# Performance work log

Measured on AMD Instinct MI355X. Metric: run time of the kernel, lower is better.

## Reference

```python
import jax, jax.numpy as jnp
import numpy as np

B, CIN, HALF, H, W = 4, 3, 32, 512, 512
K_MODE, PAD_MODE, N_LEVELS = 11, 5, 17  # 11x11 mode window, reflect pad 5, round(x*255/16) in 0..16
SLOPE, EPS = 0.01, 1e-5


def _leaky(x):
    return jnp.where(x > 0, x, SLOPE * x)


def _bn(x, g, b):
    # BatchNorm2d in training mode: batch statistics over (B,H,W), biased var
    m = x.mean(axis=(0, 2, 3), keepdims=True)
    v = x.var(axis=(0, 2, 3), keepdims=True)
    return (x - m) * jax.lax.rsqrt(v + EPS) * g[None, :, None, None] + b[None, :, None, None]


def _mode_pool(x):
    # quantize to 17 discrete levels, then sliding-window histogram mode (fused
    # equivalent of unfold + torch.mode; argmax first-hit == smallest tied value)
    k = jnp.clip(jnp.round(x * (255.0 / 16.0)), 0, N_LEVELS - 1).astype(jnp.int32)
    kp = jnp.pad(k, ((0, 0), (0, 0), (PAD_MODE, PAD_MODE), (PAD_MODE, PAD_MODE)), mode='reflect')
    onehot = (kp[..., None] == jnp.arange(N_LEVELS, dtype=jnp.int32)).astype(jnp.float32)
    counts = jax.lax.reduce_window(onehot, 0.0, jax.lax.add,
                                   (1, 1, K_MODE, K_MODE, 1), (1, 1, 1, 1, 1), 'VALID')
    mode_k = jnp.argmax(counts, axis=-1)  # [B,C,H,W]
    return mode_k.astype(jnp.float32) * (16.0 / 256.0)


def _nearest(x, Ho, Wo):
    # torch interpolate(mode='nearest'): src = floor(dst * in/out)
    hi, wi = x.shape[2], x.shape[3]
    ri = (jnp.arange(Ho) * hi) // Ho
    ci = (jnp.arange(Wo) * wi) // Wo
    return x[:, :, ri][:, :, :, ci]


def _forward(x, w1, b1, w2, b2, bn1_g, bn1_b, w3, b3, bn2_g, bn2_b,
             k_down, k_w, bnw_g, bnw_b, k_h, bnh_g, bnh_b):
    xm = _mode_pool(x)  # [B,CIN,H,W]
    # prepare: 1x1 conv -> LeakyReLU -> 1x1 conv -> BN -> LeakyReLU -> depthwise 1x1 -> BN -> LeakyReLU
    h = _leaky(jnp.einsum('bchw,oc->bohw', xm, w1) + b1[None, :, None, None])
    h = jnp.einsum('bchw,oc->bohw', h, w2) + b2[None, :, None, None]
    h = _leaky(_bn(h, bn1_g, bn1_b))
    h = h * w3[None, :, None, None] + b3[None, :, None, None]  # groups=half 1x1 conv
    h = _leaky(_bn(h, bn2_g, bn2_b))
    Bs, half, Ho, Wo = h.shape
    score = jnp.zeros((Bs, 2 * half, Ho, Wo), jnp.float32)
    d = h
    while min(d.shape[2], d.shape[3]) >= 3:  # static pyramid: 512->171->57->19->7->3->1
        d = jax.lax.conv_general_dilated(d, k_down, (3, 3), ((1, 1), (1, 1)),
                                         dimension_numbers=('NCHW', 'OIHW', 'NCHW'),
                                         feature_group_count=half)
        z = _nearest(d, Ho, Wo)
        wbr = _leaky(_bn(z * k_w[None, :, None, None], bnw_g, bnw_b))  # width branch (SharedConv k=1, no bias)
        hbr = _leaky(_bn(z * k_h[None, :, None, None], bnh_g, bnh_b))  # height branch
        # stack(dim=1).reshape => width channels first, then height channels
        score = score + jnp.concatenate([wbr, hbr], axis=1)
    return score


def setup_inputs():
    key = jax.random.key(0)
    ks = jax.random.split(key, 8)
    x = jax.random.uniform(ks[0], (B, CIN, H, W), dtype=jnp.float32)
    s1, s2 = 1.0 / np.sqrt(CIN), 1.0 / np.sqrt(2 * CIN)
    return {
        'x': x,
        'w1': jax.random.uniform(ks[1], (2 * CIN, CIN), jnp.float32, -s1, s1),
        'b1': jax.random.uniform(ks[2], (2 * CIN,), jnp.float32, -s1, s1),
        'w2': jax.random.uniform(ks[3], (HALF, 2 * CIN), jnp.float32, -s2, s2),
        'b2': jax.random.uniform(ks[4], (HALF,), jnp.float32, -s2, s2),
        'bn1_g': jnp.ones((HALF,), jnp.float32),
        'bn1_b': jnp.zeros((HALF,), jnp.float32),
        'w3': jax.random.uniform(ks[5], (HALF,), jnp.float32, -1.0, 1.0),
        'b3': jax.random.uniform(ks[6], (HALF,), jnp.float32, -1.0, 1.0),
        'bn2_g': jnp.ones((HALF,), jnp.float32),
        'bn2_b': jnp.zeros((HALF,), jnp.float32),
        'k_down': jnp.full((HALF, 1, 3, 3), 0.5, jnp.float32),  # SharedConv init
        'k_w': jnp.full((HALF,), 0.5, jnp.float32),
        'bnw_g': jnp.ones((HALF,), jnp.float32),
        'bnw_b': jnp.zeros((HALF,), jnp.float32),
        'k_h': jnp.full((HALF,), 0.5, jnp.float32),
        'bnh_g': jnp.ones((HALF,), jnp.float32),
        'bnh_b': jnp.zeros((HALF,), jnp.float32),
    }


def reference(x, w1, b1, w2, b2, bn1_g, bn1_b, w3, b3, bn2_g, bn2_b,
              k_down, k_w, bnw_g, bnw_b, k_h, bnh_g, bnh_b):
    return _forward(x, w1, b1, w2, b2, bn1_g, bn1_b, w3, b3, bn2_g, bn2_b,
                    k_down, k_w, bnw_g, bnw_b, k_h, bnh_g, bnh_b)
```

## Files before the change

kernel.cpp:

```cpp
#include <hip/hip_runtime.h>

#define HH 512
#define WW 512
#define HW 262144
#define NPIX 1048576
#define NPIXF 1048576.0f

typedef float f4 __attribute__((ext_vector_type(4)));

__device__ __forceinline__ float leaky(float v) { return v > 0.f ? v : 0.01f * v; }

__device__ __forceinline__ float repw(int i, int s) {
    return (float)(((i + 1) * 512 + s - 1) / s - (i * 512 + s - 1) / s);
}

__device__ __forceinline__ void hins(unsigned long long& h0, unsigned long long& h1,
                                     unsigned& c16, int val) {
    unsigned long long inc = 1ull << ((val & 7) * 8);
    h0 += (val < 8) ? inc : 0;
    h1 += (val >= 8 && val < 16) ? inc : 0;
    c16 += (unsigned)(val >> 4);
}
__device__ __forceinline__ void hrem(unsigned long long& h0, unsigned long long& h1,
                                     unsigned& c16, int val) {
    unsigned long long inc = 1ull << ((val & 7) * 8);
    h0 -= (val < 8) ? inc : 0;
    h1 -= (val >= 8 && val < 16) ? inc : 0;
    c16 -= (unsigned)(val >> 4);
}

__global__ __launch_bounds__(256) void mode_kernel(const float* __restrict__ x,
                                                   unsigned char* __restrict__ modeq) {
    __shared__ unsigned char q[26 * 272];
    __shared__ unsigned ch[2][267 * 5];
    const int plane = blockIdx.z;
    const int tc0 = blockIdx.x * 256;
    const int tr0 = blockIdx.y * 16;
    const float* xp = x + (size_t)plane * HW;
    for (int idx = threadIdx.x; idx < 26 * 266; idx += 256) {
        int r = idx / 266;
        int cc = idx - r * 266;
        int gr = tr0 + r - 5; gr = gr < 0 ? -gr : (gr > 511 ? 1022 - gr : gr);
        int gc = tc0 + cc - 5; gc = gc < 0 ? -gc : (gc > 511 ? 1022 - gc : gc);
        float v = rintf(xp[gr * WW + gc] * 15.9375f);
        v = fminf(fmaxf(v, 0.f), 16.f);
        q[r * 272 + cc] = (unsigned char)(int)v;
    }
    const int t = threadIdx.x;
    unsigned long long A0 = 0, A1 = 0; unsigned A2 = 0;
    unsigned long long B0 = 0, B1 = 0; unsigned B2 = 0;
    __syncthreads();
    for (int r = 0; r < 16; ++r) {
        if (r == 0) {
            #pragma unroll
            for (int v = 0; v < 11; ++v) {
                hins(A0, A1, A2, q[v * 272 + t]);
                if (t < 10) hins(B0, B1, B2, q[v * 272 + 256 + t]);
            }
        } else {
            hrem(A0, A1, A2, q[(r - 1) * 272 + t]);
            hins(A0, A1, A2, q[(r + 10) * 272 + t]);
            if (t < 10) {
                hrem(B0, B1, B2, q[(r - 1) * 272 + 256 + t]);
                hins(B0, B1, B2, q[(r + 10) * 272 + 256 + t]);
            }
        }
        unsigned* cb = ch[r & 1];
        cb[t * 5 + 0] = (unsigned)A0;
        cb[t * 5 + 1] = (unsigned)(A0 >> 32);
        cb[t * 5 + 2] = (unsigned)A1;
        cb[t * 5 + 3] = (unsigned)(A1 >> 32);
        cb[t * 5 + 4] = A2;
        if (t < 10) {
            cb[(256 + t) * 5 + 0] = (unsigned)B0;
            cb[(256 + t) * 5 + 1] = (unsigned)(B0 >> 32);
            cb[(256 + t) * 5 + 2] = (unsigned)B1;
            cb[(256 + t) * 5 + 3] = (unsigned)(B1 >> 32);
            cb[(256 + t) * 5 + 4] = B2;
        }
        __syncthreads();
        unsigned long long H0 = 0, H1 = 0; unsigned C = 0;
        #pragma unroll
        for (int v = 0; v < 11; ++v) {
            const unsigned* p = &cb[(t + v) * 5];
            H0 += (unsigned long long)p[0] | ((unsigned long long)p[1] << 32);
            H1 += (unsigned long long)p[2] | ((unsigned long long)p[3] << 32);
            C += p[4];
        }
        unsigned m = 0;
        #pragma unroll
        for (int i = 0; i < 8; ++i) {
            unsigned cnt = (unsigned)(H0 >> (8 * i)) & 0xFFu;
            unsigned val = (cnt << 8) | (unsigned)(16 - i);
            m = m > val ? m : val;
        }
        #pragma unroll
        for (int i = 8; i < 16; ++i) {
            unsigned cnt = (unsigned)(H1 >> (8 * (i - 8))) & 0xFFu;
            unsigned val = (cnt << 8) | (unsigned)(16 - i);
            m = m > val ? m : val;
        }
        unsigned val16 = (C << 8);
        m = m > val16 ? m : val16;
        int k = 16 - (int)(m & 0xFFu);
        modeq[(size_t)plane * HW + (size_t)(tr0 + r) * WW + tc0 + t] = (unsigned char)k;
    }
}

__global__ __launch_bounds__(256) void hist_kernel(const unsigned char* __restrict__ modeq,
                                                   const float* __restrict__ w1,
                                                   const float* __restrict__ b1,
                                                   unsigned* __restrict__ partial,
                                                   float* __restrict__ mom) {
    __shared__ unsigned lh[4913];
    __shared__ float mred[27][4];
    for (int i = threadIdx.x; i < 4913; i += 256) lh[i] = 0;
    __syncthreads();
    int base = blockIdx.x * 8192;
    int b = base >> 18;
    int hw0 = base & (HW - 1);
    const unsigned char* mp = modeq + (size_t)b * 3 * HW;
    #pragma unroll
    for (int j = 0; j < 8; ++j) {
        int g = threadIdx.x + 256 * j;
        int hw = hw0 + g * 4;
        unsigned u0 = *(const unsigned*)(mp + hw);
        unsigned u1 = *(const unsigned*)(mp + hw + HW);
        unsigned u2 = *(const unsigned*)(mp + hw + 2 * HW);
        #pragma unroll
        for (int k = 0; k < 4; ++k) {
            int k0 = (u0 >> (8 * k)) & 0xFF;
            int k1 = (u1 >> (8 * k)) & 0xFF;
            int k2 = (u2 >> (8 * k)) & 0xFF;
            atomicAdd(&lh[k0 + 17 * k1 + 289 * k2], 1u);
        }
    }
    __syncthreads();
    unsigned* pp = partial + blockIdx.x * 4913;
    for (int i = threadIdx.x; i < 4913; i += 256) pp[i] = lh[i];
    float w1r[18], b1r[6];
    #pragma unroll
    for (int k = 0; k < 18; ++k) w1r[k] = w1[k];
    #pragma unroll
    for (int o = 0; o < 6; ++o) b1r[o] = b1[o];
    float M[27];
    #pragma unroll
    for (int i = 0; i < 27; ++i) M[i] = 0.f;
    for (int bin = threadIdx.x; bin < 4913; bin += 256) {
        float cnt = (float)lh[bin];
        int k0 = bin % 17;
        int r = bin / 17;
        int k1 = r % 17;
        int k2 = r / 17;
        float xm0 = k0 * 0.0625f, xm1 = k1 * 0.0625f, xm2 = k2 * 0.0625f;
        float t1[6];
        #pragma unroll
        for (int o = 0; o < 6; ++o)
            t1[o] = leaky(xm0 * w1r[o * 3] + xm1 * w1r[o * 3 + 1] + xm2 * w1r[o * 3 + 2] + b1r[o]);
        #pragma unroll
        for (int o = 0; o < 6; ++o) M[o] += cnt * t1[o];
        int ii = 6;
        #pragma unroll
        for (int j = 0; j < 6; ++j)
            #pragma unroll
            for (int k = j; k < 6; ++k) { M[ii] += cnt * t1[j] * t1[k]; ++ii; }
    }
    int wv = threadIdx.x >> 6;
    #pragma unroll
    for (int i = 0; i < 27; ++i) {
        float v = M[i];
        #pragma unroll
        for (int off = 32; off >= 1; off >>= 1) v += __shfl_xor(v, off);
        if ((threadIdx.x & 63) == 0) mred[i][wv] = v;
    }
    __syncthreads();
    if (threadIdx.x < 27)
        atomicAdd(&mom[threadIdx.x],
                  mred[threadIdx.x][0] + mred[threadIdx.x][1] +
                  mred[threadIdx.x][2] + mred[threadIdx.x][3]);
}

__global__ __launch_bounds__(256) void redhist_kernel(const unsigned* __restrict__ partial,
                                                      float* __restrict__ histf) {
    int bin = blockIdx.x * 256 + threadIdx.x;
    if (bin >= 4913) return;
    unsigned s = 0;
    for (int blk = 0; blk < 128; ++blk) s += partial[blk * 4913 + bin];
    histf[bin] = (float)s;
}

__global__ void solveA_kernel(const float* __restrict__ mom, const float* __restrict__ w2,
                              const float* __restrict__ b2, const float* __restrict__ g1,
                              const float* __restrict__ bb1, float* __restrict__ p1) {
    int c = threadIdx.x;
    float w2r[6];
    #pragma unroll
    for (int k = 0; k < 6; ++k) w2r[k] = w2[c * 6 + k];
    float b2c = b2[c];
    float wm1 = 0.f;
    #pragma unroll
    for (int k = 0; k < 6; ++k) wm1 += w2r[k] * mom[k];
    float q = 0.f;
    int ii = 6;
    #pragma unroll
    for (int j = 0; j < 6; ++j)
        #pragma unroll
        for (int k = j; k < 6; ++k) {
            float f = w2r[j] * w2r[k] * mom[ii];
            q += (j == k) ? f : 2.f * f;
            ++ii;
        }
    float mean = b2c + wm1 / NPIXF;
    float ex2 = b2c * b2c + 2.f * b2c * (wm1 / NPIXF) + q / NPIXF;
    float var = ex2 - mean * mean;
    float a = g1[c] * rsqrtf(var + 1e-5f);
    p1[c] = a;
    p1[32 + c] = bb1[c] - mean * a;
}

__global__ __launch_bounds__(256) void solveB_kernel(const float* __restrict__ histf,
                                                     const float* __restrict__ w1,
                                                     const float* __restrict__ b1,
                                                     const float* __restrict__ w2,
                                                     const float* __restrict__ b2,
                                                     const float* __restrict__ p1,
                                                     float* __restrict__ tstats) {
    __shared__ float rs[8][32], rq[8][32];
    int c = threadIdx.x & 31;
    int sub = threadIdx.x >> 5;
    float w1r[18], b1r[6];
    #pragma unroll
    for (int k = 0; k < 18; ++k) w1r[k] = w1[k];
    #pragma unroll
    for (int o = 0; o < 6; ++o) b1r[o] = b1[o];
    float w2r[6];
    #pragma unroll
    for (int k = 0; k < 6; ++k) w2r[k] = w2[c * 6 + k];
    float b2c = b2[c];
    float a1 = p1[c], c1 = p1[32 + c];
    float sm = 0.f, sq = 0.f;
    for (int bin = blockIdx.x + 32 * sub; bin < 4913; bin += 256) {
        float cnt = histf[bin];
        int k0 = bin % 17;
        int r = bin / 17;
        int k1 = r % 17;
        int k2 = r / 17;
        float xm0 = k0 * 0.0625f, xm1 = k1 * 0.0625f, xm2 = k2 * 0.0625f;
        float t1[6];
        #pragma unroll
        for (int o = 0; o < 6; ++o)
            t1[o] = leaky(xm0 * w1r[o * 3] + xm1 * w1r[o * 3 + 1] + xm2 * w1r[o * 3 + 2] + b1r[o]);
        float h2 = b2c;
        #pragma unroll
        for (int k = 0; k < 6; ++k) h2 += w2r[k] * t1[k];
        float t = leaky(a1 * h2 + c1);
        sm += cnt * t;
        sq += cnt * t * t;
    }
    rs[sub][c] = sm; rq[sub][c] = sq;
    __syncthreads();
    if (threadIdx.x < 32) {
        float s = 0.f, qq = 0.f;
        #pragma unroll
        for (int g = 0; g < 8; ++g) { s += rs[g][threadIdx.x]; qq += rq[g][threadIdx.x]; }
        atomicAdd(&tstats[threadIdx.x], s);
        atomicAdd(&tstats[32 + threadIdx.x], qq);
    }
}

__global__ void fin2_kernel(const float* __restrict__ tstats, const float* __restrict__ w3,
                            const float* __restrict__ b3, const float* __restrict__ g,
                            const float* __restrict__ bb, float* __restrict__ p2) {
    int c = threadIdx.x;
    float mt = tstats[c] / NPIXF;
    float vt = tstats[32 + c] / NPIXF - mt * mt;
    float m2 = w3[c] * mt + b3[c];
    float v2 = w3[c] * w3[c] * vt;
    float a = g[c] * rsqrtf(v2 + 1e-5f);
    p2[c] = a;
    p2[32 + c] = bb[c] - m2 * a;
}

__global__ __launch_bounds__(64) void d1_kernel(const unsigned char* __restrict__ modeq,
                                                const float* __restrict__ w1,
                                                const float* __restrict__ b1,
                                                const float* __restrict__ w2,
                                                const float* __restrict__ b2,
                                                const float* __restrict__ w3,
                                                const float* __restrict__ b3,
                                                const float* __restrict__ p1,
                                                const float* __restrict__ p2,
                                                const float* __restrict__ kd,
                                                float* __restrict__ d1) {
    int j = blockIdx.x * 64 + threadIdx.x;
    if (j >= 171) return;
    int i = blockIdx.y;
    int b = blockIdx.z;
    float acc[32];
    #pragma unroll
    for (int c = 0; c < 32; ++c) acc[c] = 0.f;
    const unsigned char* mp = modeq + (size_t)b * 3 * HW;
    #pragma unroll
    for (int u = 0; u < 3; ++u) {
        int r = 3 * i - 1 + u;
        if (r < 0 || r > 511) continue;
        #pragma unroll
        for (int v = 0; v < 3; ++v) {
            int col = 3 * j - 1 + v;
            if (col < 0 || col > 511) continue;
            int off = r * WW + col;
            float xm0 = mp[off] * 0.0625f, xm1 = mp[off + HW] * 0.0625f, xm2 = mp[off + 2 * HW] * 0.0625f;
            float t1[6];
            #pragma unroll
            for (int o = 0; o < 6; ++o)
                t1[o] = leaky(xm0 * w1[o * 3] + xm1 * w1[o * 3 + 1] + xm2 * w1[o * 3 + 2] + b1[o]);
            #pragma unroll
            for (int c = 0; c < 32; ++c) {
                float h2 = b2[c];
                #pragma unroll
                for (int k = 0; k < 6; ++k) h2 += w2[c * 6 + k] * t1[k];
                float t = leaky(h2 * p1[c] + p1[32 + c]);
                float uu = t * w3[c] + b3[c];
                float hv = leaky(uu * p2[c] + p2[32 + c]);
                acc[c] += hv * kd[c * 9 + u * 3 + v];
            }
        }
    }
    size_t base = ((size_t)(b * 32) * 171 + i) * 171 + j;
    #pragma unroll
    for (int c = 0; c < 32; ++c) d1[base + (size_t)c * 29241] = acc[c];
}

__device__ __forceinline__ void red_atomic(float sm, float sq, float* rsc,
                                           float* lst, int c) {
    #pragma unroll
    for (int off = 32; off >= 1; off >>= 1) {
        sm += __shfl_xor(sm, off);
        sq += __shfl_xor(sq, off);
    }
    __syncthreads();
    int wv = threadIdx.x >> 6;
    if ((threadIdx.x & 63) == 0) { rsc[wv] = sm; rsc[8 + wv] = sq; }
    __syncthreads();
    if (threadIdx.x == 0) {
        atomicAdd(&lst[c], rsc[0] + rsc[1] + rsc[2] + rsc[3]);
        atomicAdd(&lst[32 + c], rsc[8] + rsc[9] + rsc[10] + rsc[11]);
    }
}

__device__ __forceinline__ void lvl(const float* src, int sin, float* dstL,
                                    float* dstG, int sout, const float* kreg,
                                    float* rsc, float* lst, int c) {
    float sm = 0.f, sq = 0.f;
    int n = sout * sout;
    for (int i = threadIdx.x; i < n; i += 256) {
        int oi = i / sout, oj = i - oi * sout;
        float acc = 0.f;
        #pragma unroll
        for (int u = 0; u < 3; ++u) {
            int r = 3 * oi - 1 + u;
            if ((unsigned)r >= (unsigned)sin) continue;
            #pragma unroll
            for (int v = 0; v < 3; ++v) {
                int cc = 3 * oj - 1 + v;
                if ((unsigned)cc >= (unsigned)sin) continue;
                acc += src[r * sin + cc] * kreg[u * 3 + v];
            }
        }
        dstG[i] = acc;
        if (dstL) dstL[i] = acc;
        float w = repw(oi, sout) * repw(oj, sout);
        sm += w * acc;
        sq += w * acc * acc;
    }
    red_atomic(sm, sq, rsc, lst, c);
}

__global__ __launch_bounds__(256) void pyramid_kernel(const float* __restrict__ d1,
                                                      float* __restrict__ d2,
                                                      float* __restrict__ d3,
                                                      float* __restrict__ d4,
                                                      float* __restrict__ d5,
                                                      float* __restrict__ d6,
                                                      const float* __restrict__ kd,
                                                      float* __restrict__ lstats) {
    __shared__ float buf2[3249];
    __shared__ float buf3[361];
    __shared__ float buf4[49];
    __shared__ float buf5[9];
    __shared__ float rsc[16];
    int bc = blockIdx.x;
    int c = bc & 31;
    float kreg[9];
    #pragma unroll
    for (int qq = 0; qq < 9; ++qq) kreg[qq] = kd[c * 9 + qq];
    const float* s1 = d1 + (size_t)bc * 29241;
    float sm = 0.f, sq = 0.f;
    for (int i = threadIdx.x; i < 29241; i += 256) {
        int oi = i / 171, oj = i - oi * 171;
        float w = repw(oi, 171) * repw(oj, 171);
        float v = s1[i];
        sm += w * v;
        sq += w * v * v;
    }
    red_atomic(sm, sq, rsc, &lstats[0 * 64], c);
    lvl(s1, 171, buf2, d2 + (size_t)bc * 3249, 57, kreg, rsc, &lstats[1 * 64], c);
    lvl(buf2, 57, buf3, d3 + (size_t)bc * 361, 19, kreg, rsc, &lstats[2 * 64], c);
    lvl(buf3, 19, buf4, d4 + (size_t)bc * 49, 7, kreg, rsc, &lstats[3 * 64], c);
    lvl(buf4, 7, buf5, d5 + (size_t)bc * 9, 3, kreg, rsc, &lstats[4 * 64], c);
    lvl(buf5, 3, nullptr, d6 + bc, 1, kreg, rsc, &lstats[5 * 64], c);
}

__global__ void fin3_kernel(const float* __restrict__ lstats, const float* __restrict__ kw,
                            const float* __restrict__ gw, const float* __restrict__ bw,
                            const float* __restrict__ kh, const float* __restrict__ gh,
                            const float* __restrict__ bh, float* __restrict__ lp) {
    int t = threadIdx.x;
    if (t >= 192) return;
    int l = t >> 5, c = t & 31;
    float mz = lstats[l * 64 + c] / NPIXF;
    float vz = lstats[l * 64 + 32 + c] / NPIXF - mz * mz;
    float kwc = kw[c];
    float aw = gw[c] * rsqrtf(kwc * kwc * vz + 1e-5f);
    float khc = kh[c];
    float ah = gh[c] * rsqrtf(khc * khc * vz + 1e-5f);
    float* o = lp + (size_t)(l * 32 + c) * 4;
    o[0] = kwc * aw;
    o[1] = bw[c] - kwc * mz * aw;
    o[2] = khc * ah;
    o[3] = bh[c] - khc * mz * ah;
}

__global__ __launch_bounds__(256) void final_kernel(const float* __restrict__ d1,
                                                    const float* __restrict__ d2,
                                                    const float* __restrict__ d3,
                                                    const float* __restrict__ d4,
                                                    const float* __restrict__ d5,
                                                    const float* __restrict__ d6,
                                                    const float* __restrict__ lp,
                                                    float* __restrict__ out) {
    int idx = blockIdx.x * 256 + threadIdx.x;
    int w4 = (idx & 127) << 2;
    int h = (idx >> 7) & 511;
    int c = (idx >> 16) & 31;
    int b = idx >> 21;
    const float* ds[6] = {d1, d2, d3, d4, d5, d6};
    const int ss[6] = {171, 57, 19, 7, 3, 1};
    float accw[4] = {0.f, 0.f, 0.f, 0.f};
    float acch[4] = {0.f, 0.f, 0.f, 0.f};
    #pragma unroll
    for (int l = 0; l < 6; ++l) {
        int s = ss[l];
        int sh = (h * s) >> 9;
        const float* base = ds[l] + ((size_t)(b * 32 + c) * s + sh) * s;
        const float* a = lp + (size_t)(l * 32 + c) * 4;
        float a0 = a[0], a1 = a[1], a2 = a[2], a3 = a[3];
        #pragma unroll
        for (int k = 0; k < 4; ++k) {
            int sw = ((w4 + k) * s) >> 9;
            float val = base[sw];
            accw[k] += leaky(val * a0 + a1);
            acch[k] += leaky(val * a2 + a3);
        }
    }
    size_t o = (((size_t)(b * 64 + c)) << 18) + ((size_t)h << 9) + w4;
    f4 vw = {accw[0], accw[1], accw[2], accw[3]};
    f4 vh = {acch[0], acch[1], acch[2], acch[3]};
    __builtin_nontemporal_store(vw, (f4*)(out + o));
    __builtin_nontemporal_store(vh, (f4*)(out + o + (((size_t)32) << 18)));
}

extern "C" void kernel_launch(void* const* d_in, const int* in_sizes, int n_in,
                              void* d_out, int out_size, void* d_ws, size_t ws_size,
                              hipStream_t stream) {
    const float* x     = (const float*)d_in[0];
    const float* w1    = (const float*)d_in[1];
    const float* b1    = (const float*)d_in[2];
    const float* w2    = (const float*)d_in[3];
    const float* b2    = (const float*)d_in[4];
    const float* bn1g  = (const float*)d_in[5];
    const float* bn1b  = (const float*)d_in[6];
    const float* w3    = (const float*)d_in[7];
    const float* b3    = (const float*)d_in[8];
    const float* bn2g  = (const float*)d_in[9];
    const float* bn2b  = (const float*)d_in[10];
    const float* kd    = (const float*)d_in[11];
    const float* kw    = (const float*)d_in[12];
    const float* bnwg  = (const float*)d_in[13];
    const float* bnwb  = (const float*)d_in[14];
    const float* kh    = (const float*)d_in[15];
    const float* bnhg  = (const float*)d_in[16];
    const float* bnhb  = (const float*)d_in[17];
    float* out = (float*)d_out;

    char* ws = (char*)d_ws;
    unsigned char* modeq = (unsigned char*)ws;
    float* lstats = (float*)(ws + 3145728);
    float* mom    = lstats + 384;
    float* tstats = mom + 32;
    float* p1 = (float*)(ws + 3145728 + 2048);
    float* p2 = p1 + 64;
    float* lp = p2 + 64;
    unsigned* partial = (unsigned*)(ws + 3151360);
    float* histf = (float*)(ws + 3151360 + 2515456);
    float* d1 = (float*)(ws + 3151360 + 2515456 + 20480);
    float* d2 = d1 + 3742848;
    float* d3 = d2 + 415872;
    float* d4 = d3 + 46208;
    float* d5 = d4 + 6272;
    float* d6 = d5 + 1152;

    hipMemsetAsync(lstats, 0, 2048, stream);

    mode_kernel<<<dim3(2, 32, 12), 256, 0, stream>>>(x, modeq);
    hist_kernel<<<128, 256, 0, stream>>>(modeq, w1, b1, partial, mom);
    redhist_kernel<<<20, 256, 0, stream>>>(partial, histf);
    solveA_kernel<<<1, 32, 0, stream>>>(mom, w2, b2, bn1g, bn1b, p1);
    solveB_kernel<<<32, 256, 0, stream>>>(histf, w1, b1, w2, b2, p1, tstats);
    fin2_kernel<<<1, 32, 0, stream>>>(tstats, w3, b3, bn2g, bn2b, p2);
    d1_kernel<<<dim3(3, 171, 4), 64, 0, stream>>>(modeq, w1, b1, w2, b2, w3, b3, p1, p2, kd, d1);
    pyramid_kernel<<<128, 256, 0, stream>>>(d1, d2, d3, d4, d5, d6, kd, lstats);
    fin3_kernel<<<1, 192, 0, stream>>>(lstats, kw, bnwg, bnwb, kh, bnhg, bnhb, lp);
    final_kernel<<<32768, 256, 0, stream>>>(d1, d2, d3, d4, d5, d6, lp, out);
}
```

Before: 469.6 us.

## Fuse joint histogram into mode kernel and replace atomics with partial buffers

The mode kernel now handles all three channels of a batch tile in one block. It builds the 3-channel joint histogram and first-moment partials directly, which removes the separate hist and redhist kernels and the re-read of modeq. Global float atomics and the memset are replaced by per-block partial buffers that are reduced in solveA, solveB, fin2 and fin3. The trade-off is that the mode kernel grid shrinks threefold with serial per-plane work, reducing parallelism and occupancy.

```diff
diff --git a/kernel.cpp b/kernel.cpp
--- a/kernel.cpp
+++ b/kernel.cpp
@@ -30,114 +30,105 @@
 }
 
 __global__ __launch_bounds__(256) void mode_kernel(const float* __restrict__ x,
-                                                   unsigned char* __restrict__ modeq) {
-    __shared__ unsigned char q[26 * 272];
-    __shared__ unsigned ch[2][267 * 5];
-    const int plane = blockIdx.z;
-    const int tc0 = blockIdx.x * 256;
-    const int tr0 = blockIdx.y * 16;
-    const float* xp = x + (size_t)plane * HW;
-    for (int idx = threadIdx.x; idx < 26 * 266; idx += 256) {
-        int r = idx / 266;
-        int cc = idx - r * 266;
-        int gr = tr0 + r - 5; gr = gr < 0 ? -gr : (gr > 511 ? 1022 - gr : gr);
-        int gc = tc0 + cc - 5; gc = gc < 0 ? -gc : (gc > 511 ? 1022 - gc : gc);
-        float v = rintf(xp[gr * WW + gc] * 15.9375f);
-        v = fminf(fmaxf(v, 0.f), 16.f);
-        q[r * 272 + cc] = (unsigned char)(int)v;
-    }
-    const int t = threadIdx.x;
-    unsigned long long A0 = 0, A1 = 0; unsigned A2 = 0;
-    unsigned long long B0 = 0, B1 = 0; unsigned B2 = 0;
-    __syncthreads();
-    for (int r = 0; r < 16; ++r) {
-        if (r == 0) {
-            #pragma unroll
-            for (int v = 0; v < 11; ++v) {
-                hins(A0, A1, A2, q[v * 272 + t]);
-                if (t < 10) hins(B0, B1, B2, q[v * 272 + 256 + t]);
-            }
-        } else {
-            hrem(A0, A1, A2, q[(r - 1) * 272 + t]);
-            hins(A0, A1, A2, q[(r + 10) * 272 + t]);
-            if (t < 10) {
-                hrem(B0, B1, B2, q[(r - 1) * 272 + 256 + t]);
-                hins(B0, B1, B2, q[(r + 10) * 272 + 256 + t]);
-            }
-        }
-        unsigned* cb = ch[r & 1];
-        cb[t * 5 + 0] = (unsigned)A0;
-        cb[t * 5 + 1] = (unsigned)(A0 >> 32);
-        cb[t * 5 + 2] = (unsigned)A1;
-        cb[t * 5 + 3] = (unsigned)(A1 >> 32);
-        cb[t * 5 + 4] = A2;
-        if (t < 10) {
-            cb[(256 + t) * 5 + 0] = (unsigned)B0;
-            cb[(256 + t) * 5 + 1] = (unsigned)(B0 >> 32);
-            cb[(256 + t) * 5 + 2] = (unsigned)B1;
-            cb[(256 + t) * 5 + 3] = (unsigned)(B1 >> 32);
-            cb[(256 + t) * 5 + 4] = B2;
-        }
-        __syncthreads();
-        unsigned long long H0 = 0, H1 = 0; unsigned C = 0;
-        #pragma unroll
-        for (int v = 0; v < 11; ++v) {
-            const unsigned* p = &cb[(t + v) * 5];
-            H0 += (unsigned long long)p[0] | ((unsigned long long)p[1] << 32);
-            H1 += (unsigned long long)p[2] | ((unsigned long long)p[3] << 32);
-            C += p[4];
-        }
-        unsigned m = 0;
-        #pragma unroll
-        for (int i = 0; i < 8; ++i) {
-            unsigned cnt = (unsigned)(H0 >> (8 * i)) & 0xFFu;
-            unsigned val = (cnt << 8) | (unsigned)(16 - i);
-            m = m > val ? m : val;
-        }
-        #pragma unroll
-        for (int i = 8; i < 16; ++i) {
-            unsigned cnt = (unsigned)(H1 >> (8 * (i - 8))) & 0xFFu;
-            unsigned val = (cnt << 8) | (unsigned)(16 - i);
-            m = m > val ? m : val;
-        }
-        unsigned val16 = (C << 8);
-        m = m > val16 ? m : val16;
-        int k = 16 - (int)(m & 0xFFu);
-        modeq[(size_t)plane * HW + (size_t)(tr0 + r) * WW + tc0 + t] = (unsigned char)k;
-    }
-}
-
-__global__ __launch_bounds__(256) void hist_kernel(const unsigned char* __restrict__ modeq,
+                                                   unsigned char* __restrict__ modeq,
                                                    const float* __restrict__ w1,
                                                    const float* __restrict__ b1,
                                                    unsigned* __restrict__ partial,
-                                                   float* __restrict__ mom) {
+                                                   float* __restrict__ mpart) {
+    __shared__ unsigned char q[26 * 272];
+    __shared__ unsigned ch[2][267 * 5];
     __shared__ unsigned lh[4913];
     __shared__ float mred[27][4];
-    for (int i = threadIdx.x; i < 4913; i += 256) lh[i] = 0;
-    __syncthreads();
-    int base = blockIdx.x * 8192;
-    int b = base >> 18;
-    int hw0 = base & (HW - 1);
-    const unsigned char* mp = modeq + (size_t)b * 3 * HW;
-    #pragma unroll
-    for (int j = 0; j < 8; ++j) {
-        int g = threadIdx.x + 256 * j;
-        int hw = hw0 + g * 4;
-        unsigned u0 = *(const unsigned*)(mp + hw);
-        unsigned u1 = *(const unsigned*)(mp + hw + HW);
-        unsigned u2 = *(const unsigned*)(mp + hw + 2 * HW);
-        #pragma unroll
-        for (int k = 0; k < 4; ++k) {
-            int k0 = (u0 >> (8 * k)) & 0xFF;
-            int k1 = (u1 >> (8 * k)) & 0xFF;
-            int k2 = (u2 >> (8 * k)) & 0xFF;
-            atomicAdd(&lh[k0 + 17 * k1 + 289 * k2], 1u);
+    const int t = threadIdx.x;
+    for (int i = t; i < 4913; i += 256) lh[i] = 0;
+    const int tc0 = blockIdx.x * 256;
+    const int tr0 = blockIdx.y * 16;
+    const int bb = blockIdx.z;
+    unsigned rp[3][4];
+    for (int p = 0; p < 3; ++p) {
+        const float* xp = x + (size_t)(bb * 3 + p) * HW;
+        for (int idx = t; idx < 26 * 266; idx += 256) {
+            int r = idx / 266;
+            int cc = idx - r * 266;
+            int gr = tr0 + r - 5; gr = gr < 0 ? -gr : (gr > 511 ? 1022 - gr : gr);
+            int gc = tc0 + cc - 5; gc = gc < 0 ? -gc : (gc > 511 ? 1022 - gc : gc);
+            float v = rintf(xp[gr * WW + gc] * 15.9375f);
+            v = fminf(fmaxf(v, 0.f), 16.f);
+            q[r * 272 + cc] = (unsigned char)(int)v;
         }
-    }
-    __syncthreads();
-    unsigned* pp = partial + blockIdx.x * 4913;
-    for (int i = threadIdx.x; i < 4913; i += 256) pp[i] = lh[i];
+        unsigned long long A0 = 0, A1 = 0; unsigned A2 = 0;
+        unsigned long long B0 = 0, B1 = 0; unsigned B2 = 0;
+        unsigned wkw[4] = {0u, 0u, 0u, 0u};
+        __syncthreads();
+        for (int r = 0; r < 16; ++r) {
+            if (r == 0) {
+                #pragma unroll
+                for (int v = 0; v < 11; ++v) {
+                    hins(A0, A1, A2, q[v * 272 + t]);
+                    if (t < 10) hins(B0, B1, B2, q[v * 272 + 256 + t]);
+                }
+            } else {
+                hrem(A0, A1, A2, q[(r - 1) * 272 + t]);
+                hins(A0, A1, A2, q[(r + 10) * 272 + t]);
+                if (t < 10) {
+                    hrem(B0, B1, B2, q[(r - 1) * 272 + 256 + t]);
+                    hins(B0, B1, B2, q[(r + 10) * 272 + 256 + t]);
+                }
+            }
+            unsigned* cb = ch[r & 1];
+            cb[t * 5 + 0] = (unsigned)A0;
+            cb[t * 5 + 1] = (unsigned)(A0 >> 32);
+            cb[t * 5 + 2] = (unsigned)A1;
+            cb[t * 5 + 3] = (unsigned)(A1 >> 32);
+            cb[t * 5 + 4] = A2;
+            if (t < 10) {
+                cb[(256 + t) * 5 + 0] = (unsigned)B0;
+                cb[(256 + t) * 5 + 1] = (unsigned)(B0 >> 32);
+                cb[(256 + t) * 5 + 2] = (unsigned)B1;
+                cb[(256 + t) * 5 + 3] = (unsigned)(B1 >> 32);
+                cb[(256 + t) * 5 + 4] = B2;
+            }
+            __syncthreads();
+            unsigned long long H0 = 0, H1 = 0; unsigned C = 0;
+            #pragma unroll
+            for (int v = 0; v < 11; ++v) {
+                const unsigned* pk = &cb[(t + v) * 5];
+                H0 += (unsigned long long)pk[0] | ((unsigned long long)pk[1] << 32);
+                H1 += (unsigned long long)pk[2] | ((unsigned long long)pk[3] << 32);
+                C += pk[4];
+            }
+            unsigned m = 0;
+            #pragma unroll
+            for (int i = 0; i < 8; ++i) {
+                unsigned cnt = (unsigned)(H0 >> (8 * i)) & 0xFFu;
+                unsigned val = (cnt << 8) | (unsigned)(16 - i);
+                m = m > val ? m : val;
+            }
+            #pragma unroll
+            for (int i = 8; i < 16; ++i) {
+                unsigned cnt = (unsigned)(H1 >> (8 * (i - 8))) & 0xFFu;
+                unsigned val = (cnt << 8) | (unsigned)(16 - i);
+                m = m > val ? m : val;
+            }
+            unsigned val16 = (C << 8);
+            m = m > val16 ? m : val16;
+            int k = 16 - (int)(m & 0xFFu);
+            wkw[r >> 2] |= (unsigned)k << ((r & 3) * 8);
+            modeq[(size_t)(bb * 3 + p) * HW + (size_t)(tr0 + r) * WW + tc0 + t] = (unsigned char)k;
+        }
+        rp[p][0] = wkw[0]; rp[p][1] = wkw[1]; rp[p][2] = wkw[2]; rp[p][3] = wkw[3];
+    }
+    #pragma unroll
+    for (int r = 0; r < 16; ++r) {
+        int sh = (r & 3) * 8;
+        int k0 = (rp[0][r >> 2] >> sh) & 0xFF;
+        int k1 = (rp[1][r >> 2] >> sh) & 0xFF;
+        int k2 = (rp[2][r >> 2] >> sh) & 0xFF;
+        atomicAdd(&lh[k0 + 17 * k1 + 289 * k2], 1u);
+    }
+    __syncthreads();
+    const int blk = blockIdx.x + 2 * (blockIdx.y + 32 * blockIdx.z);
+    for (int i = t; i < 4913; i += 256) partial[i * 256 + blk] = lh[i];
     float w1r[18], b1r[6];
     #pragma unroll
     for (int k = 0; k < 18; ++k) w1r[k] = w1[k];
@@ -146,7 +137,7 @@
     float M[27];
     #pragma unroll
     for (int i = 0; i < 27; ++i) M[i] = 0.f;
-    for (int bin = threadIdx.x; bin < 4913; bin += 256) {
+    for (int bin = t; bin < 4913; bin += 256) {
         float cnt = (float)lh[bin];
         int k0 = bin % 17;
         int r = bin / 17;
@@ -165,66 +156,78 @@
             #pragma unroll
             for (int k = j; k < 6; ++k) { M[ii] += cnt * t1[j] * t1[k]; ++ii; }
     }
-    int wv = threadIdx.x >> 6;
+    int wv = t >> 6;
     #pragma unroll
     for (int i = 0; i < 27; ++i) {
         float v = M[i];
         #pragma unroll
         for (int off = 32; off >= 1; off >>= 1) v += __shfl_xor(v, off);
-        if ((threadIdx.x & 63) == 0) mred[i][wv] = v;
-    }
-    __syncthreads();
-    if (threadIdx.x < 27)
-        atomicAdd(&mom[threadIdx.x],
-                  mred[threadIdx.x][0] + mred[threadIdx.x][1] +
-                  mred[threadIdx.x][2] + mred[threadIdx.x][3]);
-}
-
-__global__ __launch_bounds__(256) void redhist_kernel(const unsigned* __restrict__ partial,
-                                                      float* __restrict__ histf) {
-    int bin = blockIdx.x * 256 + threadIdx.x;
-    if (bin >= 4913) return;
-    unsigned s = 0;
-    for (int blk = 0; blk < 128; ++blk) s += partial[blk * 4913 + bin];
-    histf[bin] = (float)s;
-}
-
-__global__ void solveA_kernel(const float* __restrict__ mom, const float* __restrict__ w2,
-                              const float* __restrict__ b2, const float* __restrict__ g1,
-                              const float* __restrict__ bb1, float* __restrict__ p1) {
-    int c = threadIdx.x;
-    float w2r[6];
-    #pragma unroll
-    for (int k = 0; k < 6; ++k) w2r[k] = w2[c * 6 + k];
-    float b2c = b2[c];
-    float wm1 = 0.f;
-    #pragma unroll
-    for (int k = 0; k < 6; ++k) wm1 += w2r[k] * mom[k];
-    float q = 0.f;
-    int ii = 6;
-    #pragma unroll
-    for (int j = 0; j < 6; ++j)
-        #pragma unroll
-        for (int k = j; k < 6; ++k) {
-            float f = w2r[j] * w2r[k] * mom[ii];
-            q += (j == k) ? f : 2.f * f;
-            ++ii;
-        }
-    float mean = b2c + wm1 / NPIXF;
-    float ex2 = b2c * b2c + 2.f * b2c * (wm1 / NPIXF) + q / NPIXF;
-    float var = ex2 - mean * mean;
-    float a = g1[c] * rsqrtf(var + 1e-5f);
-    p1[c] = a;
-    p1[32 + c] = bb1[c] - mean * a;
-}
-
-__global__ __launch_bounds__(256) void solveB_kernel(const float* __restrict__ histf,
+        if ((t & 63) == 0) mred[i][wv] = v;
+    }
+    __syncthreads();
+    if (t < 27)
+        mpart[blk * 27 + t] = mred[t][0] + mred[t][1] + mred[t][2] + mred[t][3];
+}
+
+__global__ __launch_bounds__(1024) void solveA_kernel(const float* __restrict__ mpart,
+                                                      const float* __restrict__ w2,
+                                                      const float* __restrict__ b2,
+                                                      const float* __restrict__ g1,
+                                                      const float* __restrict__ bb1,
+                                                      float* __restrict__ p1) {
+    __shared__ float red[32][32];
+    __shared__ float mom[27];
+    int t = threadIdx.x;
+    int i = t & 31, g = t >> 5;
+    float s = 0.f;
+    if (i < 27) {
+        #pragma unroll
+        for (int j = 0; j < 8; ++j) s += mpart[(g + 32 * j) * 27 + i];
+    }
+    red[g][i] = s;
+    __syncthreads();
+    if (t < 27) {
+        float v = 0.f;
+        #pragma unroll
+        for (int gg = 0; gg < 32; ++gg) v += red[gg][t];
+        mom[t] = v;
+    }
+    __syncthreads();
+    if (t < 32) {
+        int c = t;
+        float w2r[6];
+        #pragma unroll
+        for (int k = 0; k < 6; ++k) w2r[k] = w2[c * 6 + k];
+        float b2c = b2[c];
+        float wm1 = 0.f;
+        #pragma unroll
+        for (int k = 0; k < 6; ++k) wm1 += w2r[k] * mom[k];
+        float q = 0.f;
+        int ii = 6;
+        #pragma unroll
+        for (int j = 0; j < 6; ++j)
+            #pragma unroll
+            for (int k = j; k < 6; ++k) {
+                float f = w2r[j] * w2r[k] * mom[ii];
+                q += (j == k) ? f : 2.f * f;
+                ++ii;
+            }
+        float mean = b2c + wm1 / NPIXF;
+        float ex2 = b2c * b2c + 2.f * b2c * (wm1 / NPIXF) + q / NPIXF;
+        float var = ex2 - mean * mean;
+        float a = g1[c] * rsqrtf(var + 1e-5f);
+        p1[c] = a;
+        p1[32 + c] = bb1[c] - mean * a;
+    }
+}
+
+__global__ __launch_bounds__(256) void solveB_kernel(const unsigned* __restrict__ partial,
                                                      const float* __restrict__ w1,
                                                      const float* __restrict__ b1,
                                                      const float* __restrict__ w2,
                                                      const float* __restrict__ b2,
                                                      const float* __restrict__ p1,
-                                                     float* __restrict__ tstats) {
+                                                     float* __restrict__ tpart) {
     __shared__ float rs[8][32], rq[8][32];
     int c = threadIdx.x & 31;
     int sub = threadIdx.x >> 5;
@@ -240,7 +243,13 @@
     float a1 = p1[c], c1 = p1[32 + c];
     float sm = 0.f, sq = 0.f;
     for (int bin = blockIdx.x + 32 * sub; bin < 4913; bin += 256) {
-        float cnt = histf[bin];
+        unsigned cs = 0;
+        const unsigned* pb = partial + (size_t)bin * 256;
+        #pragma unroll
+        for (int j = 0; j < 8; ++j) cs += pb[c + 32 * j];
+        #pragma unroll
+        for (int off = 16; off >= 1; off >>= 1) cs += __shfl_xor((int)cs, off);
+        float cnt = (float)cs;
         int k0 = bin % 17;
         int r = bin / 17;
         int k1 = r % 17;
@@ -263,17 +272,20 @@
         float s = 0.f, qq = 0.f;
         #pragma unroll
         for (int g = 0; g < 8; ++g) { s += rs[g][threadIdx.x]; qq += rq[g][threadIdx.x]; }
-        atomicAdd(&tstats[threadIdx.x], s);
-        atomicAdd(&tstats[32 + threadIdx.x], qq);
-    }
-}
-
-__global__ void fin2_kernel(const float* __restrict__ tstats, const float* __restrict__ w3,
+        tpart[blockIdx.x * 64 + threadIdx.x] = s;
+        tpart[blockIdx.x * 64 + 32 + threadIdx.x] = qq;
+    }
+}
+
+__global__ void fin2_kernel(const float* __restrict__ tpart, const float* __restrict__ w3,
                             const float* __restrict__ b3, const float* __restrict__ g,
                             const float* __restrict__ bb, float* __restrict__ p2) {
     int c = threadIdx.x;
-    float mt = tstats[c] / NPIXF;
-    float vt = tstats[32 + c] / NPIXF - mt * mt;
+    float s = 0.f, qq = 0.f;
+    #pragma unroll
+    for (int k = 0; k < 32; ++k) { s += tpart[k * 64 + c]; qq += tpart[k * 64 + 32 + c]; }
+    float mt = s / NPIXF;
+    float vt = qq / NPIXF - mt * mt;
     float m2 = w3[c] * mt + b3[c];
     float v2 = w3[c] * w3[c] * vt;
     float a = g[c] * rsqrtf(v2 + 1e-5f);
@@ -331,8 +343,7 @@
     for (int c = 0; c < 32; ++c) d1[base + (size_t)c * 29241] = acc[c];
 }
 
-__device__ __forceinline__ void red_atomic(float sm, float sq, float* rsc,
-                                           float* lst, int c) {
+__device__ __forceinline__ void red_store(float sm, float sq, float* rsc, float* ps) {
     #pragma unroll
     for (int off = 32; off >= 1; off >>= 1) {
         sm += __shfl_xor(sm, off);
@@ -343,14 +354,14 @@
     if ((threadIdx.x & 63) == 0) { rsc[wv] = sm; rsc[8 + wv] = sq; }
     __syncthreads();
     if (threadIdx.x == 0) {
-        atomicAdd(&lst[c], rsc[0] + rsc[1] + rsc[2] + rsc[3]);
-        atomicAdd(&lst[32 + c], rsc[8] + rsc[9] + rsc[10] + rsc[11]);
+        ps[0] = rsc[0] + rsc[1] + rsc[2] + rsc[3];
+        ps[1] = rsc[8] + rsc[9] + rsc[10] + rsc[11];
     }
 }
 
 __device__ __forceinline__ void lvl(const float* src, int sin, float* dstL,
                                     float* dstG, int sout, const float* kreg,
-                                    float* rsc, float* lst, int c) {
+                                    float* rsc, float* ps) {
     float sm = 0.f, sq = 0.f;
     int n = sout * sout;
     for (int i = threadIdx.x; i < n; i += 256) {
@@ -373,7 +384,7 @@
         sm += w * acc;
         sq += w * acc * acc;
     }
-    red_atomic(sm, sq, rsc, lst, c);
+    red_store(sm, sq, rsc, ps);
 }
 
 __global__ __launch_bounds__(256) void pyramid_kernel(const float* __restrict__ d1,
@@ -383,7 +394,7 @@
                                                       float* __restrict__ d5,
                                                       float* __restrict__ d6,
                                                       const float* __restrict__ kd,
-                                                      float* __restrict__ lstats) {
+                                                      float* __restrict__ pstats) {
     __shared__ float buf2[3249];
     __shared__ float buf3[361];
     __shared__ float buf4[49];
@@ -394,6 +405,7 @@
     float kreg[9];
     #pragma unroll
     for (int qq = 0; qq < 9; ++qq) kreg[qq] = kd[c * 9 + qq];
+    float* ps = pstats + (size_t)bc * 12;
     const float* s1 = d1 + (size_t)bc * 29241;
     float sm = 0.f, sq = 0.f;
     for (int i = threadIdx.x; i < 29241; i += 256) {
@@ -403,23 +415,30 @@
         sm += w * v;
         sq += w * v * v;
     }
-    red_atomic(sm, sq, rsc, &lstats[0 * 64], c);
-    lvl(s1, 171, buf2, d2 + (size_t)bc * 3249, 57, kreg, rsc, &lstats[1 * 64], c);
-    lvl(buf2, 57, buf3, d3 + (size_t)bc * 361, 19, kreg, rsc, &lstats[2 * 64], c);
-    lvl(buf3, 19, buf4, d4 + (size_t)bc * 49, 7, kreg, rsc, &lstats[3 * 64], c);
-    lvl(buf4, 7, buf5, d5 + (size_t)bc * 9, 3, kreg, rsc, &lstats[4 * 64], c);
-    lvl(buf5, 3, nullptr, d6 + bc, 1, kreg, rsc, &lstats[5 * 64], c);
-}
-
-__global__ void fin3_kernel(const float* __restrict__ lstats, const float* __restrict__ kw,
+    red_store(sm, sq, rsc, ps + 0);
+    lvl(s1, 171, buf2, d2 + (size_t)bc * 3249, 57, kreg, rsc, ps + 2);
+    lvl(buf2, 57, buf3, d3 + (size_t)bc * 361, 19, kreg, rsc, ps + 4);
+    lvl(buf3, 19, buf4, d4 + (size_t)bc * 49, 7, kreg, rsc, ps + 6);
+    lvl(buf4, 7, buf5, d5 + (size_t)bc * 9, 3, kreg, rsc, ps + 8);
+    lvl(buf5, 3, nullptr, d6 + bc, 1, kreg, rsc, ps + 10);
+}
+
+__global__ void fin3_kernel(const float* __restrict__ pstats, const float* __restrict__ kw,
                             const float* __restrict__ gw, const float* __restrict__ bw,
                             const float* __restrict__ kh, const float* __restrict__ gh,
                             const float* __restrict__ bh, float* __restrict__ lp) {
     int t = threadIdx.x;
     if (t >= 192) return;
     int l = t >> 5, c = t & 31;
-    float mz = lstats[l * 64 + c] / NPIXF;
-    float vz = lstats[l * 64 + 32 + c] / NPIXF - mz * mz;
+    float sm = 0.f, sq = 0.f;
+    #pragma unroll
+    for (int b = 0; b < 4; ++b) {
+        const float* ps = pstats + (size_t)(b * 32 + c) * 12 + 2 * l;
+        sm += ps[0];
+        sq += ps[1];
+    }
+    float mz = sm / NPIXF;
+    float vz = sq / NPIXF - mz * mz;
     float kwc = kw[c];
     float aw = gw[c] * rsqrtf(kwc * kwc * vz + 1e-5f);
     float khc = kh[c];
@@ -495,31 +514,26 @@
 
     char* ws = (char*)d_ws;
     unsigned char* modeq = (unsigned char*)ws;
-    float* lstats = (float*)(ws + 3145728);
-    float* mom    = lstats + 384;
-    float* tstats = mom + 32;
-    float* p1 = (float*)(ws + 3145728 + 2048);
+    float* mpart  = (float*)(ws + 3145728);
+    float* tpart  = (float*)(ws + 3145728 + 27648);
+    float* pstats = (float*)(ws + 3145728 + 27648 + 8192);
+    float* p1 = (float*)(ws + 3187712);
     float* p2 = p1 + 64;
     float* lp = p2 + 64;
-    unsigned* partial = (unsigned*)(ws + 3151360);
-    float* histf = (float*)(ws + 3151360 + 2515456);
-    float* d1 = (float*)(ws + 3151360 + 2515456 + 20480);
+    unsigned* partial = (unsigned*)(ws + 3191296);
+    float* d1 = (float*)(ws + 3191296 + 5030912);
     float* d2 = d1 + 3742848;
     float* d3 = d2 + 415872;
     float* d4 = d3 + 46208;
     float* d5 = d4 + 6272;
     float* d6 = d5 + 1152;
 
-    hipMemsetAsync(lstats, 0, 2048, stream);
-
-    mode_kernel<<<dim3(2, 32, 12), 256, 0, stream>>>(x, modeq);
-    hist_kernel<<<128, 256, 0, stream>>>(modeq, w1, b1, partial, mom);
-    redhist_kernel<<<20, 256, 0, stream>>>(partial, histf);
-    solveA_kernel<<<1, 32, 0, stream>>>(mom, w2, b2, bn1g, bn1b, p1);
-    solveB_kernel<<<32, 256, 0, stream>>>(histf, w1, b1, w2, b2, p1, tstats);
-    fin2_kernel<<<1, 32, 0, stream>>>(tstats, w3, b3, bn2g, bn2b, p2);
+    mode_kernel<<<dim3(2, 32, 4), 256, 0, stream>>>(x, modeq, w1, b1, partial, mpart);
+    solveA_kernel<<<1, 1024, 0, stream>>>(mpart, w2, b2, bn1g, bn1b, p1);
+    solveB_kernel<<<32, 256, 0, stream>>>(partial, w1, b1, w2, b2, p1, tpart);
+    fin2_kernel<<<1, 32, 0, stream>>>(tpart, w3, b3, bn2g, bn2b, p2);
     d1_kernel<<<dim3(3, 171, 4), 64, 0, stream>>>(modeq, w1, b1, w2, b2, w3, b3, p1, p2, kd, d1);
-    pyramid_kernel<<<128, 256, 0, stream>>>(d1, d2, d3, d4, d5, d6, kd, lstats);
-    fin3_kernel<<<1, 192, 0, stream>>>(lstats, kw, bnwg, bnwb, kh, bnhg, bnhb, lp);
+    pyramid_kernel<<<128, 256, 0, stream>>>(d1, d2, d3, d4, d5, d6, kd, pstats);
+    fin3_kernel<<<1, 192, 0, stream>>>(pstats, kw, bnwg, bnwb, kh, bnhg, bnhb, lp);
     final_kernel<<<32768, 256, 0, stream>>>(d1, d2, d3, d4, d5, d6, lp, out);
 }
```

After: 504.4 us. 1.07x slower.
